# Performance work log

Hardware: AMD Instinct MI355X
Metric: run time of the kernel (lower is better)

## Reference

```python
import jax, jax.numpy as jnp
import numpy as np

B, C, OUT, H, W = 4, 64, 64, 128, 128
K = 3
K2 = K * K  # 9 kernel sample points


def conv3x3(x, w, b):
    # stride 1, padding 1 == SAME for k=3
    y = jax.lax.conv_general_dilated(x, w, (1, 1), 'SAME',
                                     dimension_numbers=('NCHW', 'OIHW', 'NCHW'))
    return y + b[None, :, None, None]


def lrelu(v):
    return jnp.where(v >= 0, v, 0.1 * v)


def dcn_core(x, offset, mask, w, b):
    # Modulated deformable conv v2: stride 1, pad 1, dilation 1, 1 deformable group.
    # offset: [B, 2*K2, H, W] (first K2 = dy, last K2 = dx); mask: [B, K2, H, W]
    B_, C_, H_, W_ = x.shape
    oy = offset[:, :K2]
    ox = offset[:, K2:]
    ky = jnp.repeat(jnp.arange(K), K).astype(x.dtype)  # [9] kernel row offsets
    kx = jnp.tile(jnp.arange(K), K).astype(x.dtype)    # [9] kernel col offsets
    gy = jnp.arange(H_, dtype=x.dtype)
    gx = jnp.arange(W_, dtype=x.dtype)
    # sampling positions per output pixel / kernel point: [B, K2, H, W]
    py = gy[None, None, :, None] - 1.0 + ky[None, :, None, None] + oy
    px = gx[None, None, None, :] - 1.0 + kx[None, :, None, None] + ox
    y0 = jnp.floor(py)
    x0 = jnp.floor(px)
    ly = py - y0
    lx = px - x0
    xf = x.reshape(B_, C_, H_ * W_)

    def gather(yi, xi):
        valid = (yi >= 0) & (yi <= H_ - 1) & (xi >= 0) & (xi <= W_ - 1)
        yc = jnp.clip(yi, 0, H_ - 1).astype(jnp.int32)
        xc = jnp.clip(xi, 0, W_ - 1).astype(jnp.int32)
        idx = (yc * W_ + xc).reshape(B_, -1)  # [B, K2*H*W]
        vals = jax.vmap(lambda xb, ib: xb[:, ib])(xf, idx)  # [B, C, K2*H*W]
        vals = vals.reshape(B_, C_, K2, H_, W_)
        return vals * valid.reshape(B_, 1, K2, H_, W_).astype(x.dtype)

    acc = gather(y0, x0) * ((1 - ly) * (1 - lx))[:, None]
    acc = acc + gather(y0, x0 + 1) * ((1 - ly) * lx)[:, None]
    acc = acc + gather(y0 + 1, x0) * (ly * (1 - lx))[:, None]
    acc = acc + gather(y0 + 1, x0 + 1) * (ly * lx)[:, None]
    acc = acc * mask[:, None]  # [B, C, K2, H, W]
    out = jnp.einsum('bckhw,ock->bohw', acc, w.reshape(w.shape[0], C_, K2))
    return out + b[None, :, None, None]


def setup_inputs() -> dict:
    key = jax.random.key(0)
    ks = jax.random.split(key, 16)

    def wt(k, shape):
        fan_in = int(np.prod(shape[1:]))
        return jax.random.normal(k, shape, jnp.float32) * (1.0 / np.sqrt(fan_in))

    return {
        'x': jax.random.normal(ks[0], (B, C, H, W), jnp.float32),
        'x_neigh': jax.random.normal(ks[1], (B, C, H, W), jnp.float32),
        'offset_t': jax.random.normal(ks[2], (B, C, H, W), jnp.float32),
        'w_off1': wt(ks[3], (C, 2 * C, K, K)), 'b_off1': jnp.zeros((C,), jnp.float32),
        'w_off2': wt(ks[4], (C, 2 * C, K, K)), 'b_off2': jnp.zeros((C,), jnp.float32),
        'w_off3': wt(ks[5], (C, C, K, K)), 'b_off3': jnp.zeros((C,), jnp.float32),
        'w_om': wt(ks[6], (3 * K2, C, K, K)) * 0.1, 'b_om': jnp.zeros((3 * K2,), jnp.float32),
        'w_dcn': wt(ks[7], (C, C, K, K)), 'b_dcn': jnp.zeros((C,), jnp.float32),
        'w_out': wt(ks[8], (OUT, C, K, K)), 'b_out': jnp.zeros((OUT,), jnp.float32),
    }


def reference(x, x_neigh, offset_t, w_off1, b_off1, w_off2, b_off2,
              w_off3, b_off3, w_om, b_om, w_dcn, b_dcn, w_out, b_out):
    offset_1 = lrelu(conv3x3(jnp.concatenate([x, x_neigh], axis=1), w_off1, b_off1))
    offset_2 = lrelu(conv3x3(jnp.concatenate([offset_1, offset_t], axis=1), w_off2, b_off2))
    offset = lrelu(conv3x3(offset_2, w_off3, b_off3))
    # DCNv2 pack with extra_offset_mask: offset/mask predicted from `offset` features
    om = conv3x3(offset, w_om, b_om)  # [B, 3*K2, H, W]
    o1, o2, m = jnp.split(om, 3, axis=1)
    dcn_offset = jnp.concatenate([o1, o2], axis=1)
    m = jax.nn.sigmoid(m)
    align_feats = dcn_core(x, dcn_offset, m, w_dcn, b_dcn)
    align_feats = jax.nn.relu(conv3x3(align_feats, w_out, b_out))
    return (align_feats, offset)
```

## Files before the change

### kernel.cpp

```cpp
#include <hip/hip_runtime.h>
#include <hip/hip_bf16.h>
#include <math.h>

#define HH 128
#define WW 128
#define HWSZ (HH*WW)

typedef __attribute__((ext_vector_type(4))) short short4v;
typedef __attribute__((ext_vector_type(8))) short bfrag;
typedef __attribute__((ext_vector_type(4))) float f4;

__device__ inline unsigned short f2bf(float v) {
    unsigned u = __builtin_bit_cast(unsigned, v);
    unsigned r = u + 0x7fffu + ((u >> 16) & 1u);
    return (unsigned short)(r >> 16);
}
__device__ inline float bf2f(short s) {
    return __builtin_bit_cast(float, ((unsigned)(unsigned short)s) << 16);
}
__device__ inline float bf2f_lo(unsigned u) { return __builtin_bit_cast(float, u << 16); }
__device__ inline float bf2f_hi(unsigned u) { return __builtin_bit_cast(float, u & 0xffff0000u); }

__device__ inline void pack_frag(const float* __restrict__ w, short* __restrict__ dst,
                                 int i, int NIC, int NOC) {
    int j    = i & 7;
    int lane = (i >> 3) & 63;
    int f    = i >> 9;
    int tap  = f % 9;
    int g    = f / 9;
    int NCH  = NIC >> 5;
    int c32  = g % NCH;
    int oct  = g / NCH;
    int oc   = oct * 16 + (lane & 15);
    int ic   = c32 * 32 + ((lane >> 4) & 3) * 8 + j;
    float v = 0.f;
    if (oc < NOC) v = w[((size_t)oc * NIC + ic) * 9 + tap];
    dst[i] = (short)f2bf(v);
}

#define SZ128 73728
#define SZ64  36864

__global__ void pack_all_k(const float* __restrict__ w1, const float* __restrict__ w2,
                           const float* __restrict__ w3, const float* __restrict__ wom,
                           const float* __restrict__ wout, const float* __restrict__ wdcn,
                           short* __restrict__ ap)
{
    int i = blockIdx.x * 256 + threadIdx.x;
    if      (i < SZ128)                  pack_frag(w1,  ap,                          i,                    128, 64);
    else if (i < 2*SZ128)                pack_frag(w2,  ap + SZ128,                  i - SZ128,            128, 64);
    else if (i < 2*SZ128 + SZ64)         pack_frag(w3,  ap + 2*SZ128,                i - 2*SZ128,           64, 64);
    else if (i < 2*SZ128 + 2*SZ64)       pack_frag(wom, ap + 2*SZ128 + SZ64,         i - 2*SZ128 - SZ64,    64, 27);
    else if (i < 2*SZ128 + 3*SZ64)       pack_frag(wout,ap + 2*SZ128 + 2*SZ64,       i - 2*SZ128 - 2*SZ64,  64, 64);
    else if (i < 2*SZ128 + 4*SZ64)       pack_frag(wdcn,ap + 2*SZ128 + 3*SZ64,       i - 2*SZ128 - 3*SZ64,  64, 64);
}

__global__ __launch_bounds__(256) void nhwc_k(const float* __restrict__ x, short* __restrict__ xt)
{
    __shared__ short s_t[128][72];
    const int tid = threadIdx.x;
    const int h = blockIdx.x, b = blockIdx.y;
    for (int i = tid; i < 64 * 128; i += 256) {
        int c = i >> 7, w = i & 127;
        s_t[w][c] = (short)f2bf(x[((size_t)(b * 64 + c)) * HWSZ + h * WW + w]);
    }
    __syncthreads();
    for (int i = tid; i < 128 * 32; i += 256) {
        int w = i >> 5, cp = i & 31;
        unsigned pk = (unsigned)(unsigned short)s_t[w][cp * 2]
                    | ((unsigned)(unsigned short)s_t[w][cp * 2 + 1] << 16);
        *(unsigned*)&xt[(((size_t)(b * 128 + h) * 128 + w) * 64) + cp * 2] = pk;
    }
}

template<int NIC, int NOC, int OCS, int ACT, bool WH, bool WC>
__global__ __launch_bounds__(256, 4) void conv_k(
    const short* __restrict__ in1, const short* __restrict__ in2,
    const short* __restrict__ apack, const float* __restrict__ bias,
    short* __restrict__ outh, float* __restrict__ outc)
{
    constexpr int NCH = NIC / 32;
    __shared__ short s_x[3][130][40];

    const int tid  = threadIdx.x;
    const int lane = tid & 63;
    const int wv   = tid >> 6;
    const int wo   = wv & 1;
    const int wp   = wv >> 1;
    const int n16  = lane & 15;
    const int kq   = lane >> 4;
    const int h    = blockIdx.x;
    const int b    = blockIdx.y;

    f4 acc[2][4];
#pragma unroll
    for (int t = 0; t < 2; ++t)
#pragma unroll
        for (int p = 0; p < 4; ++p) acc[t][p] = (f4){0.f, 0.f, 0.f, 0.f};

    const short* a_lane = apack + (size_t)lane * 8;

    for (int cc = 0; cc < NCH; ++cc) {
        const short* src; int c0;
        if (NIC == 128 && cc >= 2) { src = in2; c0 = (cc - 2) * 32; }
        else                       { src = in1; c0 = cc * 32; }
        __syncthreads();
        for (int i = tid; i < 1560; i += 256) {
            int row = i / 520, rem = i % 520;
            int px = rem >> 2, q = rem & 3;
            int gy = h - 1 + row, gx = px - 1;
            int4 v = {0, 0, 0, 0};
            if ((unsigned)gy < 128u && (unsigned)gx < 128u)
                v = *(const int4*)&src[(((size_t)(b * 128 + gy)) * 128 + gx) * 64 + c0 + q * 8];
            *(int4*)&s_x[row][px][q * 8] = v;
        }
        __syncthreads();

        if (wo * 32 < NOC) {
#pragma unroll
            for (int tap = 0; tap < 9; ++tap) {
                const int dy = tap / 3, dx = tap % 3;
                bfrag a0 = *(const bfrag*)(a_lane + (size_t)(((wo * 2 + 0) * NCH + cc) * 9 + tap) * 512);
                bfrag a1 = *(const bfrag*)(a_lane + (size_t)(((wo * 2 + 1) * NCH + cc) * 9 + tap) * 512);
#pragma unroll
                for (int p = 0; p < 4; ++p) {
                    bfrag bb = *(const bfrag*)&s_x[dy][wp * 64 + p * 16 + n16 + dx][kq * 8];
                    acc[0][p] = __builtin_amdgcn_mfma_f32_16x16x32_bf16(a0, bb, acc[0][p], 0, 0, 0);
                    acc[1][p] = __builtin_amdgcn_mfma_f32_16x16x32_bf16(a1, bb, acc[1][p], 0, 0, 0);
                }
            }
        }
    }

#pragma unroll
    for (int oct = 0; oct < 2; ++oct) {
        int oc0 = wo * 32 + oct * 16 + kq * 4;
        if (oc0 < NOC) {
            float4 bv = *(const float4*)&bias[oc0];
#pragma unroll
            for (int p = 0; p < 4; ++p) {
                int col = wp * 64 + p * 16 + n16;
                float v0 = acc[oct][p][0] + bv.x;
                float v1 = acc[oct][p][1] + bv.y;
                float v2 = acc[oct][p][2] + bv.z;
                float v3 = acc[oct][p][3] + bv.w;
                if (ACT == 1) {
                    v0 = (v0 >= 0.f) ? v0 : 0.1f * v0;
                    v1 = (v1 >= 0.f) ? v1 : 0.1f * v1;
                    v2 = (v2 >= 0.f) ? v2 : 0.1f * v2;
                    v3 = (v3 >= 0.f) ? v3 : 0.1f * v3;
                }
                if (ACT == 2) {
                    v0 = fmaxf(v0, 0.f); v1 = fmaxf(v1, 0.f);
                    v2 = fmaxf(v2, 0.f); v3 = fmaxf(v3, 0.f);
                }
                if (WH) {
                    uint2 pk;
                    pk.x = (unsigned)f2bf(v0) | ((unsigned)f2bf(v1) << 16);
                    pk.y = (unsigned)f2bf(v2) | ((unsigned)f2bf(v3) << 16);
                    *(uint2*)&outh[(((size_t)(b * 128 + h)) * 128 + col) * OCS + oc0] = pk;
                }
                if (WC) {
                    size_t base = ((size_t)b * NOC) * HWSZ + h * WW + col;
                    outc[base + (size_t)(oc0 + 0) * HWSZ] = v0;
                    outc[base + (size_t)(oc0 + 1) * HWSZ] = v1;
                    outc[base + (size_t)(oc0 + 2) * HWSZ] = v2;
                    outc[base + (size_t)(oc0 + 3) * HWSZ] = v3;
                }
            }
        }
    }
}

__device__ inline void dcn_params(const short* __restrict__ omb, int h, int k, int tid,
                                  float (*s_pw)[4], int (*s_pi)[4])
{
    if (tid < 128) {
        int pix = tid;
        const short* o = omb + pix * 32;
        float oy = bf2f(o[k]);
        float ox = bf2f(o[9 + k]);
        float mv = bf2f(o[18 + k]);
        mv = 1.f / (1.f + expf(-mv));
        float py = (float)(h - 1 + (k / 3)) + oy;
        float px = (float)(pix - 1 + (k % 3)) + ox;
        float y0f = floorf(py), x0f = floorf(px);
        float ly = py - y0f, lx = px - x0f;
        int y0 = (int)y0f, x0 = (int)x0f;
        int y1 = y0 + 1, x1 = x0 + 1;
        float v00 = ((unsigned)y0 < 128u && (unsigned)x0 < 128u) ? 1.f : 0.f;
        float v01 = ((unsigned)y0 < 128u && (unsigned)x1 < 128u) ? 1.f : 0.f;
        float v10 = ((unsigned)y1 < 128u && (unsigned)x0 < 128u) ? 1.f : 0.f;
        float v11 = ((unsigned)y1 < 128u && (unsigned)x1 < 128u) ? 1.f : 0.f;
        int yc0 = min(max(y0, 0), 127), yc1 = min(max(y1, 0), 127);
        int xc0 = min(max(x0, 0), 127), xc1 = min(max(x1, 0), 127);
        s_pw[pix][0] = (1.f - ly) * (1.f - lx) * mv * v00;
        s_pw[pix][1] = (1.f - ly) * lx * mv * v01;
        s_pw[pix][2] = ly * (1.f - lx) * mv * v10;
        s_pw[pix][3] = ly * lx * mv * v11;
        s_pi[pix][0] = (yc0 * WW + xc0) * 64;
        s_pi[pix][1] = (yc0 * WW + xc1) * 64;
        s_pi[pix][2] = (yc1 * WW + xc0) * 64;
        s_pi[pix][3] = (yc1 * WW + xc1) * 64;
    }
}

__global__ __launch_bounds__(256, 4) void dcn_k(
    const short* __restrict__ xt, const short* __restrict__ om,
    const short* __restrict__ adcn, const float* __restrict__ bias,
    short* __restrict__ outh)
{
    __shared__ short s_samp[128][72];
    __shared__ float s_pw[128][4];
    __shared__ int   s_pi[128][4];

    const int tid  = threadIdx.x;
    const int lane = tid & 63;
    const int wv   = tid >> 6;
    const int wo   = wv & 1;
    const int wp   = wv >> 1;
    const int n16  = lane & 15;
    const int kq   = lane >> 4;
    const int h    = blockIdx.x;
    const int b    = blockIdx.y;

    f4 acc[2][4];
#pragma unroll
    for (int t = 0; t < 2; ++t)
#pragma unroll
        for (int p = 0; p < 4; ++p) acc[t][p] = (f4){0.f, 0.f, 0.f, 0.f};

    const short* a_lane = adcn + (size_t)lane * 8;
    const short* xb  = xt + (size_t)b * HWSZ * 64;
    const short* omb = om + ((size_t)(b * 128 + h)) * 128 * 32;

    dcn_params(omb, h, 0, tid, s_pw, s_pi);

    const int pp = lane >> 5;
    const int cp = lane & 31;

    for (int k = 0; k < 9; ++k) {
        __syncthreads();
#pragma unroll 4
        for (int i = 0; i < 16; ++i) {
            int pix = i * 8 + wv * 2 + pp;
            float4 w = *(const float4*)s_pw[pix];
            int4  ix = *(const int4*)s_pi[pix];
            unsigned u00 = *(const unsigned*)&xb[ix.x + cp * 2];
            unsigned u01 = *(const unsigned*)&xb[ix.y + cp * 2];
            unsigned u10 = *(const unsigned*)&xb[ix.z + cp * 2];
            unsigned u11 = *(const unsigned*)&xb[ix.w + cp * 2];
            float lo = w.x * bf2f_lo(u00) + w.y * bf2f_lo(u01) + w.z * bf2f_lo(u10) + w.w * bf2f_lo(u11);
            float hi = w.x * bf2f_hi(u00) + w.y * bf2f_hi(u01) + w.z * bf2f_hi(u10) + w.w * bf2f_hi(u11);
            *(unsigned*)&s_samp[pix][cp * 2] = (unsigned)f2bf(lo) | ((unsigned)f2bf(hi) << 16);
        }
        __syncthreads();
        if (k < 8) dcn_params(omb, h, k + 1, tid, s_pw, s_pi);
#pragma unroll
        for (int ks = 0; ks < 2; ++ks) {
            bfrag a0 = *(const bfrag*)(a_lane + (size_t)(((wo * 2 + 0) * 2 + ks) * 9 + k) * 512);
            bfrag a1 = *(const bfrag*)(a_lane + (size_t)(((wo * 2 + 1) * 2 + ks) * 9 + k) * 512);
#pragma unroll
            for (int p = 0; p < 4; ++p) {
                bfrag bb = *(const bfrag*)&s_samp[wp * 64 + p * 16 + n16][ks * 32 + kq * 8];
                acc[0][p] = __builtin_amdgcn_mfma_f32_16x16x32_bf16(a0, bb, acc[0][p], 0, 0, 0);
                acc[1][p] = __builtin_amdgcn_mfma_f32_16x16x32_bf16(a1, bb, acc[1][p], 0, 0, 0);
            }
        }
    }

#pragma unroll
    for (int oct = 0; oct < 2; ++oct) {
        int oc0 = wo * 32 + oct * 16 + kq * 4;
        float4 bv = *(const float4*)&bias[oc0];
#pragma unroll
        for (int p = 0; p < 4; ++p) {
            int col = wp * 64 + p * 16 + n16;
            uint2 pk;
            pk.x = (unsigned)f2bf(acc[oct][p][0] + bv.x) | ((unsigned)f2bf(acc[oct][p][1] + bv.y) << 16);
            pk.y = (unsigned)f2bf(acc[oct][p][2] + bv.z) | ((unsigned)f2bf(acc[oct][p][3] + bv.w) << 16);
            *(uint2*)&outh[(((size_t)(b * 128 + h)) * 128 + col) * 64 + oc0] = pk;
        }
    }
}

extern "C" void kernel_launch(void* const* d_in, const int* in_sizes, int n_in,
                              void* d_out, int out_size, void* d_ws, size_t ws_size,
                              hipStream_t stream)
{
    const float* x      = (const float*)d_in[0];
    const float* xng    = (const float*)d_in[1];
    const float* offt   = (const float*)d_in[2];
    const float* w1     = (const float*)d_in[3];
    const float* b1     = (const float*)d_in[4];
    const float* w2     = (const float*)d_in[5];
    const float* b2     = (const float*)d_in[6];
    const float* w3     = (const float*)d_in[7];
    const float* b3     = (const float*)d_in[8];
    const float* wom    = (const float*)d_in[9];
    const float* bom    = (const float*)d_in[10];
    const float* wdcn   = (const float*)d_in[11];
    const float* bdcn   = (const float*)d_in[12];
    const float* wout   = (const float*)d_in[13];
    const float* bout   = (const float*)d_in[14];

    float* out0 = (float*)d_out;
    float* out1 = out0 + (size_t)4 * 64 * HWSZ;

    const size_t NB = (size_t)4 * HWSZ * 64;
    short* xtx = (short*)d_ws;
    short* xtn = xtx + NB;
    short* xto = xtn + NB;
    short* o1  = xto + NB;
    short* apk = o1 + NB;

    short* o2    = xtn;
    short* o3    = o1;
    short* omb   = xto;
    short* align = xtn;

    short* a1p  = apk;
    short* a2p  = apk + SZ128;
    short* a3p  = apk + 2 * SZ128;
    short* aomp = apk + 2 * SZ128 + SZ64;
    short* aout = apk + 2 * SZ128 + 2 * SZ64;
    short* adcn = apk + 2 * SZ128 + 3 * SZ64;

    pack_all_k<<<(2 * SZ128 + 4 * SZ64 + 255) / 256, 256, 0, stream>>>(
        w1, w2, w3, wom, wout, wdcn, apk);
    dim3 rgrid(HH, 4);
    nhwc_k<<<rgrid, 256, 0, stream>>>(x,    xtx);
    nhwc_k<<<rgrid, 256, 0, stream>>>(xng,  xtn);
    nhwc_k<<<rgrid, 256, 0, stream>>>(offt, xto);

    conv_k<128, 64, 64, 1, true, false><<<rgrid, 256, 0, stream>>>(xtx, xtn, a1p, b1, o1, nullptr);
    conv_k<128, 64, 64, 1, true, false><<<rgrid, 256, 0, stream>>>(o1, xto, a2p, b2, o2, nullptr);
    conv_k<64, 64, 64, 1, true, true><<<rgrid, 256, 0, stream>>>(o2, nullptr, a3p, b3, o3, out1);
    conv_k<64, 27, 32, 0, true, false><<<rgrid, 256, 0, stream>>>(o3, nullptr, aomp, bom, omb, nullptr);
    dcn_k<<<rgrid, 256, 0, stream>>>(xtx, omb, adcn, bdcn, align);
    conv_k<64, 64, 64, 2, false, true><<<rgrid, 256, 0, stream>>>(align, nullptr, aout, bout, nullptr, out0);
}
```

Before: 272.6 us.

## Merge NHWC transposes, swizzle row mapping, preload weight fragments in conv and DCN

Combines the three NHWC conversion launches into one kernel indexed by tensor, which removes two launches. Conv and DCN kernels switch to a 1D grid with a swizzled row mapping so that neighbouring blocks handle rows spread across the image. Conv now hoists all nine tap weight fragments into registers before the MFMA loop, and its launch bound drops to 3 waves per EU to leave room for them. DCN double-buffers its weight fragments for the next kernel point. The extra registers reduce occupancy, and the swizzle may hurt halo locality between adjacent rows.

```diff
diff --git a/kernel.cpp b/kernel.cpp
--- a/kernel.cpp
+++ b/kernel.cpp
@@ -6,7 +6,6 @@
 #define WW 128
 #define HWSZ (HH*WW)
 
-typedef __attribute__((ext_vector_type(4))) short short4v;
 typedef __attribute__((ext_vector_type(8))) short bfrag;
 typedef __attribute__((ext_vector_type(4))) float f4;
 
@@ -55,26 +54,34 @@
     else if (i < 2*SZ128 + 4*SZ64)       pack_frag(wdcn,ap + 2*SZ128 + 3*SZ64,       i - 2*SZ128 - 3*SZ64,  64, 64);
 }
 
-__global__ __launch_bounds__(256) void nhwc_k(const float* __restrict__ x, short* __restrict__ xt)
+__global__ __launch_bounds__(256) void nhwc3_k(const float* __restrict__ x,
+                                               const float* __restrict__ xng,
+                                               const float* __restrict__ offt,
+                                               short* __restrict__ dx,
+                                               short* __restrict__ dn,
+                                               short* __restrict__ dof)
 {
     __shared__ short s_t[128][72];
     const int tid = threadIdx.x;
-    const int h = blockIdx.x, b = blockIdx.y;
+    const int h = blockIdx.x;
+    const int t = blockIdx.y >> 2, b = blockIdx.y & 3;
+    const float* src = (t == 0) ? x : (t == 1) ? xng : offt;
+    short* dst = (t == 0) ? dx : (t == 1) ? dn : dof;
     for (int i = tid; i < 64 * 128; i += 256) {
         int c = i >> 7, w = i & 127;
-        s_t[w][c] = (short)f2bf(x[((size_t)(b * 64 + c)) * HWSZ + h * WW + w]);
+        s_t[w][c] = (short)f2bf(src[((size_t)(b * 64 + c)) * HWSZ + h * WW + w]);
     }
     __syncthreads();
     for (int i = tid; i < 128 * 32; i += 256) {
         int w = i >> 5, cp = i & 31;
         unsigned pk = (unsigned)(unsigned short)s_t[w][cp * 2]
                     | ((unsigned)(unsigned short)s_t[w][cp * 2 + 1] << 16);
-        *(unsigned*)&xt[(((size_t)(b * 128 + h) * 128 + w) * 64) + cp * 2] = pk;
+        *(unsigned*)&dst[(((size_t)(b * 128 + h) * 128 + w) * 64) + cp * 2] = pk;
     }
 }
 
 template<int NIC, int NOC, int OCS, int ACT, bool WH, bool WC>
-__global__ __launch_bounds__(256, 4) void conv_k(
+__global__ __launch_bounds__(256, 3) void conv_k(
     const short* __restrict__ in1, const short* __restrict__ in2,
     const short* __restrict__ apack, const float* __restrict__ bias,
     short* __restrict__ outh, float* __restrict__ outc)
@@ -89,8 +96,10 @@
     const int wp   = wv >> 1;
     const int n16  = lane & 15;
     const int kq   = lane >> 4;
-    const int h    = blockIdx.x;
-    const int b    = blockIdx.y;
+
+    const int lin = blockIdx.x;
+    const int h   = (lin & 7) * 16 + ((lin >> 3) & 15);
+    const int b   = lin >> 7;
 
     f4 acc[2][4];
 #pragma unroll
@@ -117,16 +126,20 @@
         __syncthreads();
 
         if (wo * 32 < NOC) {
+            bfrag af0[9], af1[9];
+#pragma unroll
+            for (int tap = 0; tap < 9; ++tap) {
+                af0[tap] = *(const bfrag*)(a_lane + (size_t)(((wo * 2 + 0) * NCH + cc) * 9 + tap) * 512);
+                af1[tap] = *(const bfrag*)(a_lane + (size_t)(((wo * 2 + 1) * NCH + cc) * 9 + tap) * 512);
+            }
 #pragma unroll
             for (int tap = 0; tap < 9; ++tap) {
                 const int dy = tap / 3, dx = tap % 3;
-                bfrag a0 = *(const bfrag*)(a_lane + (size_t)(((wo * 2 + 0) * NCH + cc) * 9 + tap) * 512);
-                bfrag a1 = *(const bfrag*)(a_lane + (size_t)(((wo * 2 + 1) * NCH + cc) * 9 + tap) * 512);
 #pragma unroll
                 for (int p = 0; p < 4; ++p) {
                     bfrag bb = *(const bfrag*)&s_x[dy][wp * 64 + p * 16 + n16 + dx][kq * 8];
-                    acc[0][p] = __builtin_amdgcn_mfma_f32_16x16x32_bf16(a0, bb, acc[0][p], 0, 0, 0);
-                    acc[1][p] = __builtin_amdgcn_mfma_f32_16x16x32_bf16(a1, bb, acc[1][p], 0, 0, 0);
+                    acc[0][p] = __builtin_amdgcn_mfma_f32_16x16x32_bf16(af0[tap], bb, acc[0][p], 0, 0, 0);
+                    acc[1][p] = __builtin_amdgcn_mfma_f32_16x16x32_bf16(af1[tap], bb, acc[1][p], 0, 0, 0);
                 }
             }
         }
@@ -221,8 +234,10 @@
     const int wp   = wv >> 1;
     const int n16  = lane & 15;
     const int kq   = lane >> 4;
-    const int h    = blockIdx.x;
-    const int b    = blockIdx.y;
+
+    const int lin = blockIdx.x;
+    const int h   = (lin & 7) * 16 + ((lin >> 3) & 15);
+    const int b   = lin >> 7;
 
     f4 acc[2][4];
 #pragma unroll
@@ -238,6 +253,14 @@
 
     const int pp = lane >> 5;
     const int cp = lane & 31;
+
+    bfrag a_cur[2][2], a_nxt[2][2];
+#pragma unroll
+    for (int oi = 0; oi < 2; ++oi)
+#pragma unroll
+        for (int ks = 0; ks < 2; ++ks)
+            a_cur[oi][ks] = *(const bfrag*)(a_lane +
+                (size_t)(((wo * 2 + oi) * 2 + ks) * 9 + 0) * 512);
 
     for (int k = 0; k < 9; ++k) {
         __syncthreads();
@@ -255,18 +278,29 @@
             *(unsigned*)&s_samp[pix][cp * 2] = (unsigned)f2bf(lo) | ((unsigned)f2bf(hi) << 16);
         }
         __syncthreads();
-        if (k < 8) dcn_params(omb, h, k + 1, tid, s_pw, s_pi);
+        if (k < 8) {
+            dcn_params(omb, h, k + 1, tid, s_pw, s_pi);
+#pragma unroll
+            for (int oi = 0; oi < 2; ++oi)
+#pragma unroll
+                for (int ks = 0; ks < 2; ++ks)
+                    a_nxt[oi][ks] = *(const bfrag*)(a_lane +
+                        (size_t)(((wo * 2 + oi) * 2 + ks) * 9 + (k + 1)) * 512);
+        }
 #pragma unroll
         for (int ks = 0; ks < 2; ++ks) {
-            bfrag a0 = *(const bfrag*)(a_lane + (size_t)(((wo * 2 + 0) * 2 + ks) * 9 + k) * 512);
-            bfrag a1 = *(const bfrag*)(a_lane + (size_t)(((wo * 2 + 1) * 2 + ks) * 9 + k) * 512);
 #pragma unroll
             for (int p = 0; p < 4; ++p) {
                 bfrag bb = *(const bfrag*)&s_samp[wp * 64 + p * 16 + n16][ks * 32 + kq * 8];
-                acc[0][p] = __builtin_amdgcn_mfma_f32_16x16x32_bf16(a0, bb, acc[0][p], 0, 0, 0);
-                acc[1][p] = __builtin_amdgcn_mfma_f32_16x16x32_bf16(a1, bb, acc[1][p], 0, 0, 0);
+                acc[0][p] = __builtin_amdgcn_mfma_f32_16x16x32_bf16(a_cur[0][ks], bb, acc[0][p], 0, 0, 0);
+                acc[1][p] = __builtin_amdgcn_mfma_f32_16x16x32_bf16(a_cur[1][ks], bb, acc[1][p], 0, 0, 0);
             }
         }
+#pragma unroll
+        for (int oi = 0; oi < 2; ++oi)
+#pragma unroll
+            for (int ks = 0; ks < 2; ++ks)
+                a_cur[oi][ks] = a_nxt[oi][ks];
     }
 
 #pragma unroll
@@ -328,15 +362,12 @@
 
     pack_all_k<<<(2 * SZ128 + 4 * SZ64 + 255) / 256, 256, 0, stream>>>(
         w1, w2, w3, wom, wout, wdcn, apk);
-    dim3 rgrid(HH, 4);
-    nhwc_k<<<rgrid, 256, 0, stream>>>(x,    xtx);
-    nhwc_k<<<rgrid, 256, 0, stream>>>(xng,  xtn);
-    nhwc_k<<<rgrid, 256, 0, stream>>>(offt, xto);
-
-    conv_k<128, 64, 64, 1, true, false><<<rgrid, 256, 0, stream>>>(xtx, xtn, a1p, b1, o1, nullptr);
-    conv_k<128, 64, 64, 1, true, false><<<rgrid, 256, 0, stream>>>(o1, xto, a2p, b2, o2, nullptr);
-    conv_k<64, 64, 64, 1, true, true><<<rgrid, 256, 0, stream>>>(o2, nullptr, a3p, b3, o3, out1);
-    conv_k<64, 27, 32, 0, true, false><<<rgrid, 256, 0, stream>>>(o3, nullptr, aomp, bom, omb, nullptr);
-    dcn_k<<<rgrid, 256, 0, stream>>>(xtx, omb, adcn, bdcn, align);
-    conv_k<64, 64, 64, 2, false, true><<<rgrid, 256, 0, stream>>>(align, nullptr, aout, bout, nullptr, out0);
-}
+    nhwc3_k<<<dim3(HH, 12), 256, 0, stream>>>(x, xng, offt, xtx, xtn, xto);
+
+    conv_k<128, 64, 64, 1, true, false><<<512, 256, 0, stream>>>(xtx, xtn, a1p, b1, o1, nullptr);
+    conv_k<128, 64, 64, 1, true, false><<<512, 256, 0, stream>>>(o1, xto, a2p, b2, o2, nullptr);
+    conv_k<64, 64, 64, 1, true, true><<<512, 256, 0, stream>>>(o2, nullptr, a3p, b3, o3, out1);
+    conv_k<64, 27, 32, 0, true, false><<<512, 256, 0, stream>>>(o3, nullptr, aomp, bom, omb, nullptr);
+    dcn_k<<<512, 256, 0, stream>>>(xtx, omb, adcn, bdcn, align);
+    conv_k<64, 64, 64, 2, false, true><<<512, 256, 0, stream>>>(align, nullptr, aout, bout, nullptr, out0);
+}
```

New measurement: 249.6 us. 8.4% less time.
